# Performance work log

Measured on AMD Instinct MI355X. Metric: run time of the kernel, lower is better.

## Reference

```python
import jax, jax.numpy as jnp
import numpy as np

T, N, R = 10, 50000, 50000   # time steps, nodes per graph, total restaurants
D_IN, D, H = 128, 64, 4      # input dim, hidden dim, attention heads
E = 400000                   # edges per timestep (before self-loops)
HD = D // H                  # head dim


def setup_inputs() -> dict:
    key = jax.random.key(0)
    ks = jax.random.split(key, 16)
    inp = {}
    inp["x"] = jax.random.normal(ks[0], (T, N, D_IN), jnp.float32)
    inp["edge_index"] = jax.random.randint(ks[1], (T, 2, E), 0, N, jnp.int32)
    inp["edge_weight"] = jax.random.uniform(ks[2], (T, E), jnp.float32)
    # per-timestep permutation mapping local node idx -> global restaurant idx
    inp["global_idx"] = jax.vmap(lambda k: jax.random.permutation(k, R))(
        jax.random.split(ks[3], T)).astype(jnp.int32)
    s = 0.05
    inp["gcn1_w"] = jax.random.normal(ks[4], (D, D_IN), jnp.float32) * s
    inp["gcn1_b"] = jnp.zeros((D,), jnp.float32)
    inp["gcn2_w"] = jax.random.normal(ks[5], (D, D), jnp.float32) * s
    inp["gcn2_b"] = jnp.zeros((D,), jnp.float32)
    inp["in_proj_w"] = jax.random.normal(ks[6], (3 * D, D), jnp.float32) * s
    inp["in_proj_b"] = jnp.zeros((3 * D,), jnp.float32)
    inp["out_proj_w"] = jax.random.normal(ks[7], (D, D), jnp.float32) * s
    inp["out_proj_b"] = jnp.zeros((D,), jnp.float32)
    inp["w1"] = jnp.ones((T, D), jnp.float32)
    inp["w2"] = jnp.ones((T, D), jnp.float32)
    inp["w3"] = jnp.ones((D,), jnp.float32)
    inp["w4"] = jnp.ones((D,), jnp.float32)
    inp["ln1_g"] = jnp.ones((D,), jnp.float32)
    inp["ln1_b"] = jnp.zeros((D,), jnp.float32)
    inp["ln2_g"] = jnp.ones((D,), jnp.float32)
    inp["ln2_b"] = jnp.zeros((D,), jnp.float32)
    inp["fc_w"] = jax.random.normal(ks[8], (D, D), jnp.float32) * s
    inp["fc_b"] = jnp.zeros((D,), jnp.float32)
    return inp


def _layer_norm(x, g, b, eps=1e-5):
    mu = jnp.mean(x, axis=-1, keepdims=True)
    var = jnp.mean((x - mu) ** 2, axis=-1, keepdims=True)
    return (x - mu) * jax.lax.rsqrt(var + eps) * g + b


def _gcn_layer(h, src, dst, ew, W, b):
    # PyG GCNConv with edge weights; self-loops already appended by caller.
    deg = jax.ops.segment_sum(ew, dst, num_segments=N)
    dinv = jnp.where(deg > 0, jax.lax.rsqrt(deg), 0.0)
    norm = dinv[src] * ew * dinv[dst]                      # [E+N]
    hw = h @ W.T                                           # [N, D]
    agg = jax.ops.segment_sum(norm[:, None] * hw[src], dst, num_segments=N)
    return agg + b


def _forward(x, edge_index, edge_weight, global_idx,
             gcn1_w, gcn1_b, gcn2_w, gcn2_b,
             in_proj_w, in_proj_b, out_proj_w, out_proj_b,
             w1, w2, w3, w4, ln1_g, ln1_b, ln2_g, ln2_b, fc_w, fc_b):
    loop = jnp.arange(N, dtype=edge_index.dtype)
    src = jnp.concatenate([edge_index[:, 0], jnp.broadcast_to(loop, (T, N))], axis=1)
    dst = jnp.concatenate([edge_index[:, 1], jnp.broadcast_to(loop, (T, N))], axis=1)
    ew = jnp.concatenate([edge_weight, jnp.ones((T, N), edge_weight.dtype)], axis=1)

    def per_t(xt, st, dt, wt):
        h = jax.nn.relu(_gcn_layer(xt, st, dt, wt, gcn1_w, gcn1_b))
        return jax.nn.relu(_gcn_layer(h, st, dt, wt, gcn2_w, gcn2_b))

    feat = jax.vmap(per_t)(x, src, dst, ew)                # [T, N, D]

    # scatter local features to global alignment (permutation per timestep)
    aligned = jax.vmap(lambda g, f: jnp.zeros((R, D), f.dtype).at[g].set(f))(
        global_idx, feat)                                  # [T, R, D]
    time_embeds = jnp.transpose(aligned, (1, 0, 2))        # [R, T, D]

    presence = jax.vmap(
        lambda g: jnp.zeros((R,), bool).at[g].set(True))(global_idx)  # [T, R]
    key_padding_mask = ~presence.T                          # [R, T], True = ignore
    bias = jnp.where(key_padding_mask, -1e9, 0.0)           # [R, T]

    # multi-head self-attention over time axis (batch_first, batch = R)
    qkv = time_embeds @ in_proj_w.T + in_proj_b             # [R, T, 3D]
    q, k, v = jnp.split(qkv, 3, axis=-1)
    q = q.reshape(R, T, H, HD)
    k = k.reshape(R, T, H, HD)
    v = v.reshape(R, T, H, HD)
    scores = jnp.einsum('rthd,rshd->rhts', q, k) / np.sqrt(HD)
    scores = scores + bias[:, None, None, :]
    attn = jax.nn.softmax(scores, axis=-1)                  # [R, H, T, T]
    ao = jnp.einsum('rhts,rshd->rthd', attn, v).reshape(R, T, D)
    attn_out = ao @ out_proj_w.T + out_proj_b               # [R, T, D]

    # dropouts are identity in eval mode
    time_feat = _layer_norm(w1 * time_embeds + w2 * attn_out, ln1_g, ln1_b)
    final = time_feat[:, -1, :]                             # [R, D]
    out = final @ fc_w.T + fc_b                             # [R, D]
    return _layer_norm(w3 * final + w4 * out, ln2_g, ln2_b)


def reference(x, edge_index, edge_weight, global_idx,
              gcn1_w, gcn1_b, gcn2_w, gcn2_b,
              in_proj_w, in_proj_b, out_proj_w, out_proj_b,
              w1, w2, w3, w4, ln1_g, ln1_b, ln2_g, ln2_b, fc_w, fc_b):
    return _forward(x, edge_index, edge_weight, global_idx,
                    gcn1_w, gcn1_b, gcn2_w, gcn2_b,
                    in_proj_w, in_proj_b, out_proj_w, out_proj_b,
                    w1, w2, w3, w4, ln1_g, ln1_b, ln2_g, ln2_b, fc_w, fc_b)
```

## Files before the change

### kernel.cpp

```cpp
#include <hip/hip_runtime.h>
#include <cstdint>
#include <cstddef>

namespace {

constexpr int T = 10;
constexpr int N = 50000;
constexpr int R = 50000;
constexpr int DIN = 128;
constexpr int D = 64;
constexpr int E = 400000;

constexpr int BINS = 16384;
constexpr int NR = 4;
constexpr int SEG = 25;
constexpr int ESEG = E / SEG;
constexpr int EV4 = ESEG / 4;

constexpr float WSCALE = 262144.0f;
constexpr float WINV = 1.0f / 262144.0f;

typedef _Float16 h16;
typedef __attribute__((ext_vector_type(8))) _Float16 f16x8;
typedef __attribute__((ext_vector_type(4))) _Float16 f16x4;
typedef __attribute__((ext_vector_type(4))) float f32x4;

__global__ __launch_bounds__(256) void k_hist(const int* __restrict__ ei,
                                              const float* __restrict__ ew,
                                              unsigned* __restrict__ pu) {
  __shared__ unsigned h[BINS];
  int b = blockIdx.x;
  int s = b % SEG;
  int tr = b / SEG;
  int r = tr % NR;
  int t = tr / NR;
  for (int i = threadIdx.x; i < BINS; i += 256) h[i] = 0u;
  __syncthreads();
  int bin0 = r * BINS;
  const int4* dst4 = (const int4*)(ei + (size_t)t * 2 * E + E + s * ESEG);
  const float4* ew4 = (const float4*)(ew + (size_t)t * E + s * ESEG);
  for (int i = threadIdx.x; i < EV4; i += 256) {
    int4 d = dst4[i];
    float4 w = ew4[i];
    unsigned a0 = (unsigned)(d.x - bin0);
    unsigned a1 = (unsigned)(d.y - bin0);
    unsigned a2 = (unsigned)(d.z - bin0);
    unsigned a3 = (unsigned)(d.w - bin0);
    if (a0 < (unsigned)BINS) atomicAdd(&h[a0], 0x1000000u + (unsigned)fmaf(w.x, WSCALE, 0.5f));
    if (a1 < (unsigned)BINS) atomicAdd(&h[a1], 0x1000000u + (unsigned)fmaf(w.y, WSCALE, 0.5f));
    if (a2 < (unsigned)BINS) atomicAdd(&h[a2], 0x1000000u + (unsigned)fmaf(w.z, WSCALE, 0.5f));
    if (a3 < (unsigned)BINS) atomicAdd(&h[a3], 0x1000000u + (unsigned)fmaf(w.w, WSCALE, 0.5f));
  }
  __syncthreads();
  size_t base = (size_t)b * BINS;
  for (int i = threadIdx.x; i < BINS; i += 256) pu[base + i] = h[i];
}

__global__ __launch_bounds__(256) void k_hreduce(const unsigned* __restrict__ pu,
                                                 int* __restrict__ cnt,
                                                 float* __restrict__ dinv) {
  int i = blockIdx.x * 256 + threadIdx.x;
  if (i >= T * N) return;
  int t = i / N, n = i - t * N;
  int r = n / BINS, rel = n - r * BINS;
  unsigned c = 0;
  unsigned wsum = 0;
  #pragma unroll
  for (int s = 0; s < SEG; ++s) {
    unsigned v = pu[((size_t)((t * NR + r) * SEG + s)) * BINS + rel];
    c += v >> 24;
    wsum += v & 0xFFFFFFu;
  }
  cnt[i] = (int)c;
  dinv[i] = rsqrtf(1.0f + (float)wsum * WINV);
}

__global__ __launch_bounds__(256) void k_scan(const int* __restrict__ cnt,
                                              int* __restrict__ rowptr) {
  int t = blockIdx.x;
  int lane = threadIdx.x & 63, wid = threadIdx.x >> 6;
  __shared__ int wsum[4];
  __shared__ int carry_s;
  if (threadIdx.x == 0) carry_s = 0;
  __syncthreads();
  const int4* cp = (const int4*)(cnt + (size_t)t * N);
  int4* rp = (int4*)(rowptr + (size_t)t * N);
  constexpr int NI4 = N / 4;
  for (int base = 0; base < NI4; base += 256) {
    int i = base + threadIdx.x;
    int4 v = make_int4(0, 0, 0, 0);
    if (i < NI4) v = cp[i];
    int tot = v.x + v.y + v.z + v.w;
    int s = tot;
    #pragma unroll
    for (int off = 1; off < 64; off <<= 1) {
      int u = __shfl_up(s, off, 64);
      if (lane >= off) s += u;
    }
    if (lane == 63) wsum[wid] = s;
    int carry = carry_s;
    __syncthreads();
    int wadd = 0;
    #pragma unroll
    for (int w = 0; w < 4; ++w) if (w < wid) wadd += wsum[w];
    if (i < NI4) {
      int excl = carry + wadd + s - tot;
      int4 o;
      o.x = excl;
      o.y = excl + v.x;
      o.z = o.y + v.y;
      o.w = o.z + v.z;
      rp[i] = o;
    }
    __syncthreads();
    if (threadIdx.x == 0) carry_s = carry + wsum[0] + wsum[1] + wsum[2] + wsum[3];
    __syncthreads();
  }
}

__global__ __launch_bounds__(256) void k_segoff(unsigned* __restrict__ pu,
                                                const int* __restrict__ rowptr) {
  int i = blockIdx.x * 256 + threadIdx.x;
  if (i >= T * N) return;
  int t = i / N, n = i - t * N;
  int r = n / BINS, rel = n - r * BINS;
  unsigned run = (unsigned)rowptr[i];
  #pragma unroll
  for (int s = 0; s < SEG; ++s) {
    size_t base = ((size_t)((t * NR + r) * SEG + s)) * BINS + rel;
    unsigned v = pu[base];
    pu[base] = run;
    run += v >> 24;
  }
}

__global__ __launch_bounds__(256) void k_fill2(const int* __restrict__ ei,
                                               const float* __restrict__ ew,
                                               const unsigned* __restrict__ pu,
                                               int2* __restrict__ pk) {
  __shared__ int cur[BINS];
  int b = blockIdx.x;
  int s = b % SEG;
  int tr = b / SEG;
  int r = tr % NR;
  int t = tr / NR;
  size_t pbase = (size_t)b * BINS;
  for (int i = threadIdx.x; i < BINS; i += 256) cur[i] = (int)pu[pbase + i];
  __syncthreads();
  int bin0 = r * BINS;
  const int4* src4 = (const int4*)(ei + (size_t)t * 2 * E + s * ESEG);
  const int4* dst4 = (const int4*)(ei + (size_t)t * 2 * E + E + s * ESEG);
  const float4* ew4 = (const float4*)(ew + (size_t)t * E + s * ESEG);
  int2* pkt = pk + (size_t)t * E;
  for (int i = threadIdx.x; i < EV4; i += 256) {
    int4 d = dst4[i];
    int4 sv = src4[i];
    float4 w = ew4[i];
    unsigned a0 = (unsigned)(d.x - bin0);
    unsigned a1 = (unsigned)(d.y - bin0);
    unsigned a2 = (unsigned)(d.z - bin0);
    unsigned a3 = (unsigned)(d.w - bin0);
    if (a0 < (unsigned)BINS) {
      int pos = atomicAdd(&cur[a0], 1);
      pkt[pos] = make_int2(sv.x, __float_as_int(w.x));
    }
    if (a1 < (unsigned)BINS) {
      int pos = atomicAdd(&cur[a1], 1);
      pkt[pos] = make_int2(sv.y, __float_as_int(w.y));
    }
    if (a2 < (unsigned)BINS) {
      int pos = atomicAdd(&cur[a2], 1);
      pkt[pos] = make_int2(sv.z, __float_as_int(w.z));
    }
    if (a3 < (unsigned)BINS) {
      int pos = atomicAdd(&cur[a3], 1);
      pkt[pos] = make_int2(sv.w, __float_as_int(w.w));
    }
  }
}

__global__ __launch_bounds__(256) void k_prep(const float* __restrict__ g1w,
                                              const float* __restrict__ g2w,
                                              const float* __restrict__ inw,
                                              const float* __restrict__ outw,
                                              const float* __restrict__ fcw,
                                              h16* __restrict__ Wb) {
  int i = blockIdx.x * 256 + threadIdx.x;
  if (i >= 32768) return;
  const float* src;
  int off;
  if (i < 8192)       { src = g1w;  off = 0; }
  else if (i < 12288) { src = g2w;  off = 8192; }
  else if (i < 24576) { src = inw;  off = 12288; }
  else if (i < 28672) { src = outw; off = 24576; }
  else                { src = fcw;  off = 28672; }
  Wb[i] = (h16)src[i - off];
}

template <int K, int NT, bool F16B, int MODE>
__global__ __launch_bounds__(256) void k_mm(const h16* __restrict__ Wb,
                                            const void* __restrict__ Bv,
                                            const float* __restrict__ biasp,
                                            h16* __restrict__ out,
                                            int Mwaves) {
  int wv = threadIdx.x >> 6, lane = threadIdx.x & 63;
  int wave = blockIdx.x * 4 + wv;
  if (wave >= Mwaves) return;
  int m0 = wave * 16;
  int half = lane & 15, quad = lane >> 4;
  constexpr int KS = K / 32;
  int m = m0 + half;
  float ds = 1.0f;
  if (MODE == 2) ds = biasp[m];
  f16x8 bfrag[KS];
  if (F16B) {
    const h16* Bp = (const h16*)Bv + (size_t)m * K + quad * 8;
    #pragma unroll
    for (int ks = 0; ks < KS; ++ks) bfrag[ks] = *(const f16x8*)(Bp + ks * 32);
  } else {
    const float* Bp = (const float*)Bv + (size_t)m * K + quad * 8;
    #pragma unroll
    for (int ks = 0; ks < KS; ++ks) {
      float4 f0 = *(const float4*)(Bp + ks * 32);
      float4 f1 = *(const float4*)(Bp + ks * 32 + 4);
      f16x8 b;
      b[0] = (h16)f0.x; b[1] = (h16)f0.y; b[2] = (h16)f0.z; b[3] = (h16)f0.w;
      b[4] = (h16)f1.x; b[5] = (h16)f1.y; b[6] = (h16)f1.z; b[7] = (h16)f1.w;
      bfrag[ks] = b;
    }
  }
  #pragma unroll
  for (int jt = 0; jt < NT; ++jt) {
    f32x4 acc = {0.f, 0.f, 0.f, 0.f};
    const h16* Wp = Wb + (size_t)(jt * 16 + half) * K + quad * 8;
    #pragma unroll
    for (int ks = 0; ks < KS; ++ks) {
      f16x8 afrag = *(const f16x8*)(Wp + ks * 32);
      acc = __builtin_amdgcn_mfma_f32_16x16x32_f16(afrag, bfrag[ks], acc, 0, 0, 0);
    }
    int j = jt * 16 + quad * 4;
    if (MODE == 2) {
      acc[0] *= ds; acc[1] *= ds; acc[2] *= ds; acc[3] *= ds;
    }
    f16x4 o;
    o[0] = (h16)acc[0]; o[1] = (h16)acc[1]; o[2] = (h16)acc[2]; o[3] = (h16)acc[3];
    *(f16x4*)(out + (size_t)m * (NT * 16) + j) = o;
  }
}

template <bool SCATTER>
__global__ __launch_bounds__(256) void k_gather(
    const h16* __restrict__ hw, const int2* __restrict__ pk,
    const float* __restrict__ dinv, const int* __restrict__ rowptr,
    const int* __restrict__ cnt, const float* __restrict__ bias,
    const int* __restrict__ gidx, h16* __restrict__ outp) {
  __shared__ __align__(16) float red[4][8][68];
  int wv = threadIdx.x >> 6, lane = threadIdx.x & 63;
  int t = blockIdx.y;
  int nd = lane >> 5;
  int grp = (lane >> 3) & 3;
  int sub = lane & 7;
  int n = blockIdx.x * 8 + wv * 2 + nd;
  const h16* hwt = hw + (size_t)t * N * D;
  const int2* pkt = pk + (size_t)t * E;
  int start = rowptr[t * N + n];
  int m = cnt[t * N + n];
  int nA = blockIdx.x * 8 + wv * 2;
  int nB = nA + 1;
  float selfA = (float)hwt[(size_t)nA * D + lane];
  float selfB = (float)hwt[(size_t)nB * D + lane];
  float dnA = dinv[t * N + nA];
  float dnB = dinv[t * N + nB];
  float bi = bias[lane];
  f32x4 accL = {0.f, 0.f, 0.f, 0.f};
  f32x4 accH = {0.f, 0.f, 0.f, 0.f};
  int e = grp;
  for (; e + 4 < m; e += 8) {
    int2 ra = pkt[start + e];
    int2 rb = pkt[start + e + 4];
    float wa = __int_as_float(ra.y);
    float wb = __int_as_float(rb.y);
    f16x8 ha = *(const f16x8*)(hwt + (size_t)ra.x * D + sub * 8);
    f16x8 hb = *(const f16x8*)(hwt + (size_t)rb.x * D + sub * 8);
    #pragma unroll
    for (int j = 0; j < 4; ++j) {
      accL[j] = fmaf(wa, (float)ha[j], accL[j]);
      accH[j] = fmaf(wa, (float)ha[j + 4], accH[j]);
    }
    #pragma unroll
    for (int j = 0; j < 4; ++j) {
      accL[j] = fmaf(wb, (float)hb[j], accL[j]);
      accH[j] = fmaf(wb, (float)hb[j + 4], accH[j]);
    }
  }
  if (e < m) {
    int2 ra = pkt[start + e];
    float wa = __int_as_float(ra.y);
    f16x8 ha = *(const f16x8*)(hwt + (size_t)ra.x * D + sub * 8);
    #pragma unroll
    for (int j = 0; j < 4; ++j) {
      accL[j] = fmaf(wa, (float)ha[j], accL[j]);
      accH[j] = fmaf(wa, (float)ha[j + 4], accH[j]);
    }
  }
  float* rw = &red[wv][nd * 4 + grp][sub * 8];
  *(f32x4*)(rw) = accL;
  *(f32x4*)(rw + 4) = accH;
  __builtin_amdgcn_wave_barrier();
  #pragma unroll
  for (int d2 = 0; d2 < 2; ++d2) {
    int nn = nA + d2;
    float s = red[wv][d2 * 4 + 0][lane] + red[wv][d2 * 4 + 1][lane] +
              red[wv][d2 * 4 + 2][lane] + red[wv][d2 * 4 + 3][lane];
    float selfv = d2 ? selfB : selfA;
    float dn = d2 ? dnB : dnA;
    float v = fmaxf(fmaf(dn, s + selfv, bi), 0.f);
    size_t ro;
    if (SCATTER) {
      int rr2 = gidx[(size_t)t * R + nn];
      ro = ((size_t)rr2 * T + t) * D + lane;
    } else {
      ro = ((size_t)t * N + nn) * D + lane;
    }
    outp[ro] = (h16)v;
  }
}

constexpr int KVP = 132;
constexpr int P72 = 72;

__global__ __launch_bounds__(256) void k_tail(
    const h16* __restrict__ te,
    const h16* __restrict__ WIb,
    const float* __restrict__ inB,
    const h16* __restrict__ WOb,
    const float* __restrict__ outB,
    const h16* __restrict__ WFb,
    const float* __restrict__ fcB,
    const float* __restrict__ w1,
    const float* __restrict__ w2,
    const float* __restrict__ w3,
    const float* __restrict__ w4,
    const float* __restrict__ g1, const float* __restrict__ b1,
    const float* __restrict__ g2, const float* __restrict__ b2,
    float* __restrict__ outp) {
  __shared__ __align__(16) h16 kvl[160][KVP];
  __shared__ __align__(16) h16 ql[16][P72];
  __shared__ __align__(16) h16 aol[16][P72];
  __shared__ __align__(16) h16 tbuf[16][P72];
  __shared__ __align__(16) h16 fbuf[16][P72];
  __shared__ __align__(16) float pf[16][64];

  int wv = threadIdx.x >> 6, lane = threadIdx.x & 63;
  int half = lane & 15, quad = lane >> 4;
  int g0 = blockIdx.x * 160;

  for (int tt = wv; tt < 10; tt += 4) {
    int lr = tt * 16 + half;
    const h16* Bp = te + (size_t)(g0 + lr) * 64 + quad * 8;
    f16x8 b0 = *(const f16x8*)(Bp);
    f16x8 b1f = *(const f16x8*)(Bp + 32);
    int rloc = lr / 10;
    bool isq = (lr - rloc * 10) == 9;
    #pragma unroll
    for (int jt = 0; jt < 12; ++jt) {
      f32x4 acc = {0.f, 0.f, 0.f, 0.f};
      const h16* Wp = WIb + (size_t)(jt * 16 + half) * 64 + quad * 8;
      acc = __builtin_amdgcn_mfma_f32_16x16x32_f16(*(const f16x8*)(Wp), b0, acc, 0, 0, 0);
      acc = __builtin_amdgcn_mfma_f32_16x16x32_f16(*(const f16x8*)(Wp + 32), b1f, acc, 0, 0, 0);
      int j = jt * 16 + quad * 4;
      float4 b4 = *(const float4*)(inB + j);
      f16x4 o;
      o[0] = (h16)(acc[0] + b4.x); o[1] = (h16)(acc[1] + b4.y);
      o[2] = (h16)(acc[2] + b4.z); o[3] = (h16)(acc[3] + b4.w);
      if (jt < 4) {
        if (isq) *(f16x4*)(&ql[rloc][j]) = o;
      } else {
        *(f16x4*)(&kvl[lr][j - 64]) = o;
      }
    }
  }
  __syncthreads();

  #pragma unroll
  for (int i = 0; i < 4; ++i) {
    int rl = wv * 4 + i;
    float qv = (float)ql[rl][lane];
    float sc[T], vv[T];
    #pragma unroll
    for (int s = 0; s < T; ++s) {
      float kk = (float)kvl[rl * 10 + s][lane];
      vv[s] = (float)kvl[rl * 10 + s][64 + lane];
      float p = qv * kk;
      p += __shfl_xor(p, 8, 16);
      p += __shfl_xor(p, 4, 16);
      p += __shfl_xor(p, 2, 16);
      p += __shfl_xor(p, 1, 16);
      sc[s] = p * 0.25f;
    }
    float mx = sc[0];
    #pragma unroll
    for (int s = 1; s < T; ++s) mx = fmaxf(mx, sc[s]);
    float ssum = 0.f;
    #pragma unroll
    for (int s = 0; s < T; ++s) { sc[s] = expf(sc[s] - mx); ssum += sc[s]; }
    float rinv = 1.0f / ssum;
    float aov = 0.f;
    #pragma unroll
    for (int s = 0; s < T; ++s) aov = fmaf(sc[s] * rinv, vv[s], aov);
    aol[rl][lane] = (h16)aov;
  }
  __syncthreads();

  {
    const h16* Bp = &aol[half][quad * 8];
    f16x8 b0 = *(const f16x8*)(Bp);
    f16x8 b1f = *(const f16x8*)(Bp + 32);
    f32x4 acc = {0.f, 0.f, 0.f, 0.f};
    const h16* Wp = WOb + (size_t)(wv * 16 + half) * 64 + quad * 8;
    acc = __builtin_amdgcn_mfma_f32_16x16x32_f16(*(const f16x8*)(Wp), b0, acc, 0, 0, 0);
    acc = __builtin_amdgcn_mfma_f32_16x16x32_f16(*(const f16x8*)(Wp + 32), b1f, acc, 0, 0, 0);
    int j = wv * 16 + quad * 4;
    float4 b4 = *(const float4*)(outB + j);
    f16x4 o;
    o[0] = (h16)(acc[0] + b4.x); o[1] = (h16)(acc[1] + b4.y);
    o[2] = (h16)(acc[2] + b4.z); o[3] = (h16)(acc[3] + b4.w);
    *(f16x4*)(&tbuf[half][j]) = o;
  }
  __syncthreads();

  {
    float w1l = w1[(T - 1) * 64 + lane];
    float w2l = w2[(T - 1) * 64 + lane];
    float g1l = g1[lane], b1l = b1[lane];
    #pragma unroll
    for (int i = 0; i < 4; ++i) {
      int rl = wv * 4 + i;
      float t9 = (float)te[(size_t)(g0 + rl * 10 + 9) * 64 + lane];
      float pr = (float)tbuf[rl][lane];
      float pre = w1l * t9 + w2l * pr;
      float s1 = pre;
      #pragma unroll
      for (int off = 32; off >= 1; off >>= 1) s1 += __shfl_xor(s1, off, 64);
      float mu = s1 * (1.0f / 64.0f);
      float dv = pre - mu;
      float s2 = dv * dv;
      #pragma unroll
      for (int off = 32; off >= 1; off >>= 1) s2 += __shfl_xor(s2, off, 64);
      float rstd = 1.0f / sqrtf(s2 * (1.0f / 64.0f) + 1e-5f);
      float fin = dv * rstd * g1l + b1l;
      pf[rl][lane] = fin;
      fbuf[rl][lane] = (h16)fin;
    }
  }
  __syncthreads();

  {
    const h16* Bp = &fbuf[half][quad * 8];
    f16x8 b0 = *(const f16x8*)(Bp);
    f16x8 b1f = *(const f16x8*)(Bp + 32);
    f32x4 acc = {0.f, 0.f, 0.f, 0.f};
    const h16* Wp = WFb + (size_t)(wv * 16 + half) * 64 + quad * 8;
    acc = __builtin_amdgcn_mfma_f32_16x16x32_f16(*(const f16x8*)(Wp), b0, acc, 0, 0, 0);
    acc = __builtin_amdgcn_mfma_f32_16x16x32_f16(*(const f16x8*)(Wp + 32), b1f, acc, 0, 0, 0);
    int j = wv * 16 + quad * 4;
    float4 b4 = *(const float4*)(fcB + j);
    f16x4 o;
    o[0] = (h16)(acc[0] + b4.x); o[1] = (h16)(acc[1] + b4.y);
    o[2] = (h16)(acc[2] + b4.z); o[3] = (h16)(acc[3] + b4.w);
    *(f16x4*)(&tbuf[half][j]) = o;
  }
  __syncthreads();

  {
    float w3l = w3[lane], w4l = w4[lane];
    float g2l = g2[lane], b2l = b2[lane];
    #pragma unroll
    for (int i = 0; i < 4; ++i) {
      int rl = wv * 4 + i;
      float fin = pf[rl][lane];
      float oo = (float)tbuf[rl][lane];
      float pre = w3l * fin + w4l * oo;
      float s1 = pre;
      #pragma unroll
      for (int off = 32; off >= 1; off >>= 1) s1 += __shfl_xor(s1, off, 64);
      float mu = s1 * (1.0f / 64.0f);
      float dv = pre - mu;
      float s2 = dv * dv;
      #pragma unroll
      for (int off = 32; off >= 1; off >>= 1) s2 += __shfl_xor(s2, off, 64);
      float rstd = 1.0f / sqrtf(s2 * (1.0f / 64.0f) + 1e-5f);
      outp[(size_t)(blockIdx.x * 16 + rl) * 64 + lane] = dv * rstd * g2l + b2l;
    }
  }
}

}

extern "C" void kernel_launch(void* const* d_in, const int* in_sizes, int n_in,
                              void* d_out, int out_size, void* d_ws, size_t ws_size,
                              hipStream_t stream) {
  const float* x      = (const float*)d_in[0];
  const int*   ei     = (const int*)d_in[1];
  const float* ew     = (const float*)d_in[2];
  const int*   gidx   = (const int*)d_in[3];
  const float* gcn1_w = (const float*)d_in[4];
  const float* gcn1_b = (const float*)d_in[5];
  const float* gcn2_w = (const float*)d_in[6];
  const float* gcn2_b = (const float*)d_in[7];
  const float* in_w   = (const float*)d_in[8];
  const float* in_b   = (const float*)d_in[9];
  const float* out_w  = (const float*)d_in[10];
  const float* out_b  = (const float*)d_in[11];
  const float* w1     = (const float*)d_in[12];
  const float* w2     = (const float*)d_in[13];
  const float* w3     = (const float*)d_in[14];
  const float* w4     = (const float*)d_in[15];
  const float* ln1_g  = (const float*)d_in[16];
  const float* ln1_b  = (const float*)d_in[17];
  const float* ln2_g  = (const float*)d_in[18];
  const float* ln2_b  = (const float*)d_in[19];
  const float* fc_w   = (const float*)d_in[20];
  const float* fc_b   = (const float*)d_in[21];
  float* outp = (float*)d_out;

  char* ws = (char*)d_ws;
  size_t off = 0;
  auto alloc = [&](size_t bytes) {
    void* p = ws + off;
    off += (bytes + 255) & ~(size_t)255;
    return p;
  };
  h16* h1te = (h16*)alloc(sizeof(h16) * (size_t)T * N * D);
  h16* Wb   = (h16*)alloc(sizeof(h16) * 32768);
  float* dinv   = (float*)alloc(sizeof(float) * T * N);
  int*   cnt    = (int*)alloc(sizeof(int) * T * N);
  int*   rowptr = (int*)alloc(sizeof(int) * T * N);
  int2*  pk     = (int2*)alloc(sizeof(int2) * (size_t)T * E);
  size_t pu_off = off;
  unsigned* pu  = (unsigned*)alloc(sizeof(unsigned) * (size_t)T * NR * SEG * BINS);
  h16* hw = (h16*)(ws + pu_off);
  size_t hw_end = pu_off + sizeof(h16) * (size_t)T * N * D;
  if (hw_end > off) off = hw_end;

  const h16* W1b = Wb;
  const h16* W2b = Wb + 8192;
  const h16* WIb = Wb + 12288;
  const h16* WOb = Wb + 24576;
  const h16* WFb = Wb + 28672;

  const int M = T * N;
  const int MW = M / 16;
  const int PREP_BLOCKS = T * NR * SEG;

  k_hist<<<PREP_BLOCKS, 256, 0, stream>>>(ei, ew, pu);
  k_hreduce<<<(T * N + 255) / 256, 256, 0, stream>>>(pu, cnt, dinv);
  k_scan<<<T, 256, 0, stream>>>(cnt, rowptr);
  k_segoff<<<(T * N + 255) / 256, 256, 0, stream>>>(pu, rowptr);
  k_fill2<<<PREP_BLOCKS, 256, 0, stream>>>(ei, ew, pu, pk);
  k_prep<<<128, 256, 0, stream>>>(gcn1_w, gcn2_w, in_w, out_w, fc_w, Wb);

  dim3 gg(N / 8, T);
  k_mm<DIN, 4, false, 2><<<(MW + 3) / 4, 256, 0, stream>>>(W1b, x, dinv, hw, MW);
  k_gather<false><<<gg, 256, 0, stream>>>(hw, pk, dinv, rowptr, cnt, gcn1_b, nullptr, h1te);
  k_mm<D, 4, true, 2><<<(MW + 3) / 4, 256, 0, stream>>>(W2b, h1te, dinv, hw, MW);
  k_gather<true><<<gg, 256, 0, stream>>>(hw, pk, dinv, rowptr, cnt, gcn2_b, gidx, h1te);

  k_tail<<<R / 16, 256, 0, stream>>>(h1te, WIb, in_b, WOb, out_b, WFb, fc_b,
                                     w1, w2, w3, w4, ln1_g, ln1_b, ln2_g, ln2_b, outp);
}
```

Measured before the change: 985.7 us.

## Fuse histogram reduce, scan and segment offsets; unroll gather by four

Merges the three kernels that reduced histogram partials, prefix-scanned the counts and wrote segment offsets into one kernel. Each block scans its nodes locally and claims a base offset per timestep with an atomicAdd on a counter zeroed in k_prep, which now runs first. This removes two launches, a serial 10-block scan and a second pass over the partial histograms. The trade-off is that CSR row placement now depends on block arrival order and is nondeterministic, which stays valid because gather reads each row from rowptr and cnt. The GCN gather loop also gets a 4-edge unrolled main loop to keep more neighbour loads in flight, at some cost in register pressure.

```diff
diff --git a/kernel.cpp b/kernel.cpp
--- a/kernel.cpp
+++ b/kernel.cpp
@@ -56,81 +56,54 @@
   for (int i = threadIdx.x; i < BINS; i += 256) pu[base + i] = h[i];
 }
 
-__global__ __launch_bounds__(256) void k_hreduce(const unsigned* __restrict__ pu,
-                                                 int* __restrict__ cnt,
-                                                 float* __restrict__ dinv) {
-  int i = blockIdx.x * 256 + threadIdx.x;
-  if (i >= T * N) return;
-  int t = i / N, n = i - t * N;
-  int r = n / BINS, rel = n - r * BINS;
-  unsigned c = 0;
-  unsigned wsum = 0;
-  #pragma unroll
-  for (int s = 0; s < SEG; ++s) {
-    unsigned v = pu[((size_t)((t * NR + r) * SEG + s)) * BINS + rel];
-    c += v >> 24;
-    wsum += v & 0xFFFFFFu;
-  }
-  cnt[i] = (int)c;
-  dinv[i] = rsqrtf(1.0f + (float)wsum * WINV);
-}
-
-__global__ __launch_bounds__(256) void k_scan(const int* __restrict__ cnt,
-                                              int* __restrict__ rowptr) {
-  int t = blockIdx.x;
+__global__ __launch_bounds__(256) void k_hreduce2(unsigned* __restrict__ pu,
+                                                  int* __restrict__ cnt,
+                                                  float* __restrict__ dinv,
+                                                  int* __restrict__ rowptr,
+                                                  int* __restrict__ tbase) {
+  int t = blockIdx.y;
+  int n = blockIdx.x * 256 + threadIdx.x;
   int lane = threadIdx.x & 63, wid = threadIdx.x >> 6;
   __shared__ int wsum[4];
-  __shared__ int carry_s;
-  if (threadIdx.x == 0) carry_s = 0;
-  __syncthreads();
-  const int4* cp = (const int4*)(cnt + (size_t)t * N);
-  int4* rp = (int4*)(rowptr + (size_t)t * N);
-  constexpr int NI4 = N / 4;
-  for (int base = 0; base < NI4; base += 256) {
-    int i = base + threadIdx.x;
-    int4 v = make_int4(0, 0, 0, 0);
-    if (i < NI4) v = cp[i];
-    int tot = v.x + v.y + v.z + v.w;
-    int s = tot;
-    #pragma unroll
-    for (int off = 1; off < 64; off <<= 1) {
-      int u = __shfl_up(s, off, 64);
-      if (lane >= off) s += u;
-    }
-    if (lane == 63) wsum[wid] = s;
-    int carry = carry_s;
-    __syncthreads();
-    int wadd = 0;
-    #pragma unroll
-    for (int w = 0; w < 4; ++w) if (w < wid) wadd += wsum[w];
-    if (i < NI4) {
-      int excl = carry + wadd + s - tot;
-      int4 o;
-      o.x = excl;
-      o.y = excl + v.x;
-      o.z = o.y + v.y;
-      o.w = o.z + v.z;
-      rp[i] = o;
-    }
-    __syncthreads();
-    if (threadIdx.x == 0) carry_s = carry + wsum[0] + wsum[1] + wsum[2] + wsum[3];
-    __syncthreads();
-  }
-}
-
-__global__ __launch_bounds__(256) void k_segoff(unsigned* __restrict__ pu,
-                                                const int* __restrict__ rowptr) {
-  int i = blockIdx.x * 256 + threadIdx.x;
-  if (i >= T * N) return;
-  int t = i / N, n = i - t * N;
-  int r = n / BINS, rel = n - r * BINS;
-  unsigned run = (unsigned)rowptr[i];
+  __shared__ int base_s;
+  unsigned cs[SEG];
+  unsigned c = 0, wacc = 0;
+  bool ok = (n < N);
+  int r = 0, rel = 0;
+  if (ok) {
+    r = n / BINS; rel = n - r * BINS;
+    #pragma unroll
+    for (int s = 0; s < SEG; ++s) {
+      unsigned v = pu[((size_t)((t * NR + r) * SEG + s)) * BINS + rel];
+      cs[s] = v >> 24;
+      c += cs[s];
+      wacc += v & 0xFFFFFFu;
+    }
+    cnt[t * N + n] = (int)c;
+    dinv[t * N + n] = rsqrtf(1.0f + (float)wacc * WINV);
+  }
+  int sv = (int)c;
   #pragma unroll
-  for (int s = 0; s < SEG; ++s) {
-    size_t base = ((size_t)((t * NR + r) * SEG + s)) * BINS + rel;
-    unsigned v = pu[base];
-    pu[base] = run;
-    run += v >> 24;
+  for (int off = 1; off < 64; off <<= 1) {
+    int u = __shfl_up(sv, off, 64);
+    if (lane >= off) sv += u;
+  }
+  if (lane == 63) wsum[wid] = sv;
+  __syncthreads();
+  int wadd = 0;
+  #pragma unroll
+  for (int w = 0; w < 4; ++w) if (w < wid) wadd += wsum[w];
+  if (threadIdx.x == 255) base_s = atomicAdd(&tbase[t], wadd + sv);
+  __syncthreads();
+  if (ok) {
+    unsigned run = (unsigned)(base_s + wadd + sv - (int)c);
+    rowptr[t * N + n] = (int)run;
+    #pragma unroll
+    for (int s = 0; s < SEG; ++s) {
+      size_t b = ((size_t)((t * NR + r) * SEG + s)) * BINS + rel;
+      pu[b] = run;
+      run += cs[s];
+    }
   }
 }
 
@@ -184,9 +157,13 @@
                                               const float* __restrict__ inw,
                                               const float* __restrict__ outw,
                                               const float* __restrict__ fcw,
-                                              h16* __restrict__ Wb) {
+                                              h16* __restrict__ Wb,
+                                              int* __restrict__ tbase) {
   int i = blockIdx.x * 256 + threadIdx.x;
-  if (i >= 32768) return;
+  if (i >= 32768) {
+    if (i < 32768 + 16) tbase[i - 32768] = 0;
+    return;
+  }
   const float* src;
   int off;
   if (i < 8192)       { src = g1w;  off = 0; }
@@ -275,6 +252,40 @@
   f32x4 accL = {0.f, 0.f, 0.f, 0.f};
   f32x4 accH = {0.f, 0.f, 0.f, 0.f};
   int e = grp;
+  for (; e + 12 < m; e += 16) {
+    int2 r0 = pkt[start + e];
+    int2 r1 = pkt[start + e + 4];
+    int2 r2 = pkt[start + e + 8];
+    int2 r3 = pkt[start + e + 12];
+    float w0 = __int_as_float(r0.y);
+    float w1 = __int_as_float(r1.y);
+    float w2 = __int_as_float(r2.y);
+    float w3 = __int_as_float(r3.y);
+    f16x8 h0 = *(const f16x8*)(hwt + (size_t)r0.x * D + sub * 8);
+    f16x8 h1 = *(const f16x8*)(hwt + (size_t)r1.x * D + sub * 8);
+    f16x8 h2 = *(const f16x8*)(hwt + (size_t)r2.x * D + sub * 8);
+    f16x8 h3 = *(const f16x8*)(hwt + (size_t)r3.x * D + sub * 8);
+    #pragma unroll
+    for (int j = 0; j < 4; ++j) {
+      accL[j] = fmaf(w0, (float)h0[j], accL[j]);
+      accH[j] = fmaf(w0, (float)h0[j + 4], accH[j]);
+    }
+    #pragma unroll
+    for (int j = 0; j < 4; ++j) {
+      accL[j] = fmaf(w1, (float)h1[j], accL[j]);
+      accH[j] = fmaf(w1, (float)h1[j + 4], accH[j]);
+    }
+    #pragma unroll
+    for (int j = 0; j < 4; ++j) {
+      accL[j] = fmaf(w2, (float)h2[j], accL[j]);
+      accH[j] = fmaf(w2, (float)h2[j + 4], accH[j]);
+    }
+    #pragma unroll
+    for (int j = 0; j < 4; ++j) {
+      accL[j] = fmaf(w3, (float)h3[j], accL[j]);
+      accH[j] = fmaf(w3, (float)h3[j + 4], accH[j]);
+    }
+  }
   for (; e + 4 < m; e += 8) {
     int2 ra = pkt[start + e];
     int2 rb = pkt[start + e + 4];
@@ -533,6 +544,7 @@
   };
   h16* h1te = (h16*)alloc(sizeof(h16) * (size_t)T * N * D);
   h16* Wb   = (h16*)alloc(sizeof(h16) * 32768);
+  int* tbase = (int*)alloc(sizeof(int) * 16);
   float* dinv   = (float*)alloc(sizeof(float) * T * N);
   int*   cnt    = (int*)alloc(sizeof(int) * T * N);
   int*   rowptr = (int*)alloc(sizeof(int) * T * N);
@@ -553,12 +565,12 @@
   const int MW = M / 16;
   const int PREP_BLOCKS = T * NR * SEG;
 
+  k_prep<<<129, 256, 0, stream>>>(gcn1_w, gcn2_w, in_w, out_w, fc_w, Wb, tbase);
+
   k_hist<<<PREP_BLOCKS, 256, 0, stream>>>(ei, ew, pu);
-  k_hreduce<<<(T * N + 255) / 256, 256, 0, stream>>>(pu, cnt, dinv);
-  k_scan<<<T, 256, 0, stream>>>(cnt, rowptr);
-  k_segoff<<<(T * N + 255) / 256, 256, 0, stream>>>(pu, rowptr);
+  dim3 hg((N + 255) / 256, T);
+  k_hreduce2<<<hg, 256, 0, stream>>>(pu, cnt, dinv, rowptr, tbase);
   k_fill2<<<PREP_BLOCKS, 256, 0, stream>>>(ei, ew, pu, pk);
-  k_prep<<<128, 256, 0, stream>>>(gcn1_w, gcn2_w, in_w, out_w, fc_w, Wb);
 
   dim3 gg(N / 8, T);
   k_mm<DIN, 4, false, 2><<<(MW + 3) / 4, 256, 0, stream>>>(W1b, x, dinv, hw, MW);
```

New measurement: 978.0 us. Within noise of the previous version (-0.8%).
